# Optimization experiments

Hardware: AMD Instinct MI355X
Metric: run time of the kernel (lower is better)

The kernel has to match this reference:

```python
import jax, jax.numpy as jnp
import numpy as np

B, S, D = 4, 2048, 1024


def setup_inputs() -> dict:
    key = jax.random.key(0)
    k1, k2, k3, k4 = jax.random.split(key, 4)
    x = jax.random.normal(k1, (B, S, D), dtype=jnp.float32)
    # 'random_normal' keras initializer uses stddev=0.05
    w_keys = jax.random.normal(k2, (D, D), dtype=jnp.float32) * 0.05
    w_queries = jax.random.normal(k3, (D, D), dtype=jnp.float32) * 0.05
    w_values = jax.random.normal(k4, (D, D), dtype=jnp.float32) * 0.05
    return {"x": x, "w_keys": w_keys, "w_queries": w_queries, "w_values": w_values}


def reference(x, w_keys, w_queries, w_values):
    # fact = sqrt(input feature dim)
    fact = jnp.sqrt(jnp.asarray(x.shape[-1], x.dtype))
    vk = x @ w_keys      # [B,S,D]
    vq = x @ w_queries   # [B,S,D]
    vv = x @ w_values    # [B,S,D]
    # NOTE: module computes K @ Q^T (keys as rows), softmax over last axis
    kq = jnp.einsum('bsd,btd->bst', vk, vq) / fact   # [B,S,S]
    sn = jax.nn.softmax(kq, axis=-1)
    # pm + transpose_b cancel: out = sn @ vv
    out = jnp.einsum('bst,btd->bsd', sn, vv)         # [B,S,D]
    return out
```

## Files before the change

kernel.cpp:

```cpp
#include <hip/hip_runtime.h>


typedef __attribute__((ext_vector_type(8))) short bf16x8;
typedef __attribute__((ext_vector_type(4))) float f32x4;

__device__ __forceinline__ unsigned short f2bf(float f) {
    unsigned int u = __float_as_uint(f);
    u += 0x7fff + ((u >> 16) & 1);
    return (unsigned short)(u >> 16);
}

__device__ __forceinline__ void gld_lds16(const unsigned short* g, unsigned short* l) {
    __builtin_amdgcn_global_load_lds(
        (const __attribute__((address_space(1))) void*)g,
        (__attribute__((address_space(3))) void*)l, 16, 0, 0);
}

template<int N> __device__ __forceinline__ void vmcnt_wait() {
    if constexpr (N == 0) asm volatile("s_waitcnt vmcnt(0)" ::: "memory");
    else if constexpr (N == 8) asm volatile("s_waitcnt vmcnt(8)" ::: "memory");
}
__device__ __forceinline__ void bar() {
    asm volatile("" ::: "memory");
    __builtin_amdgcn_s_barrier();
    asm volatile("" ::: "memory");
}

template<int KT, bool RS>
__device__ __forceinline__ void gemm4(
    const unsigned short* __restrict__ A, const unsigned short* __restrict__ B,
    int lda, int ldb, int bm, int bn,
    unsigned short* As, unsigned short* Bs,
    f32x4 (&acc)[4][4], f32x4 (&os)[4])
{
    const int tid  = threadIdx.x;
    const int lane = tid & 63;
    const int wave = tid >> 6;
    const int wr = wave >> 1, wc = wave & 1;
    const int lr = lane & 15, kg = lane >> 4;

    const bf16x8 ONES = { (short)0x3F80, (short)0x3F80, (short)0x3F80, (short)0x3F80,
                          (short)0x3F80, (short)0x3F80, (short)0x3F80, (short)0x3F80 };

    const int srow = tid >> 2;
    const int ssrc = ((tid & 3) ^ ((tid >> 3) & 3)) * 8;
    const unsigned short* pa0 = A + (size_t)(bm + srow) * lda + ssrc;
    const unsigned short* pa1 = A + (size_t)(bm + 64 + srow) * lda + ssrc;
    const unsigned short* pb0 = B + (size_t)(bn + srow) * ldb + ssrc;
    const unsigned short* pb1 = B + (size_t)(bn + 64 + srow) * ldb + ssrc;

    const int phys = (kg ^ ((lr >> 1) & 3)) * 8;
    const int aoff = (wr * 64 + lr) * 32 + phys;
    const int boff = (wc * 64 + lr) * 32 + phys;

    auto stage = [&](int buf, int kt) {
        unsigned short* da = As + buf * 8192 + wave * 512;
        unsigned short* db = Bs + buf * 8192 + wave * 512;
        #pragma unroll
        for (int kh = 0; kh < 2; kh++) {
            const int go = kt * 64 + kh * 32;
            gld_lds16(pa0 + go, da + kh * 4096);
            gld_lds16(pa1 + go, da + kh * 4096 + 2048);
            gld_lds16(pb0 + go, db + kh * 4096);
            gld_lds16(pb1 + go, db + kh * 4096 + 2048);
        }
    };

    stage(0, 0);
    stage(1, 1);
    vmcnt_wait<8>();
    bar();

    for (int kt = 0; kt < KT; ++kt) {
        const int c = kt & 1;
        const unsigned short* Ab = As + c * 8192 + aoff;
        const unsigned short* Bb = Bs + c * 8192 + boff;

        #pragma unroll
        for (int kh = 0; kh < 2; kh++) {
            bf16x8 af[4], bf[4];
            #pragma unroll
            for (int mf = 0; mf < 4; mf++)
                af[mf] = *reinterpret_cast<const bf16x8*>(Ab + kh * 4096 + mf * 512);
            #pragma unroll
            for (int nf = 0; nf < 4; nf++)
                bf[nf] = *reinterpret_cast<const bf16x8*>(Bb + kh * 4096 + nf * 512);
            __builtin_amdgcn_s_setprio(1);
            #pragma unroll
            for (int mf = 0; mf < 4; mf++)
                #pragma unroll
                for (int nf = 0; nf < 4; nf++)
                    acc[mf][nf] = __builtin_amdgcn_mfma_f32_16x16x32_bf16(af[mf], bf[nf], acc[mf][nf], 0, 0, 0);
            if constexpr (RS) {
                #pragma unroll
                for (int mf = 0; mf < 4; mf++)
                    os[mf] = __builtin_amdgcn_mfma_f32_16x16x32_bf16(af[mf], ONES, os[mf], 0, 0, 0);
            }
            __builtin_amdgcn_s_setprio(0);
        }

        if (kt == KT - 1) break;
        bar();
        if (kt + 2 < KT) {
            stage(c, kt + 2);
            vmcnt_wait<8>();
        } else {
            vmcnt_wait<0>();
        }
        bar();
    }
}

__global__ __launch_bounds__(256) void stage1(
    const float* __restrict__ x,  unsigned short* __restrict__ xb,
    const float* __restrict__ wv, unsigned short* __restrict__ wvT,
    const float* __restrict__ wq, const float* __restrict__ wk,
    unsigned short* __restrict__ Gt)
{
    __shared__ unsigned short SM[4608];
    const int bid = blockIdx.x;
    const int tid = threadIdx.x;

    if (bid >= 256 && bid < 4352) {
        const size_t idx = (size_t)(bid - 256) * 256 + tid;
        const float4* xi = reinterpret_cast<const float4*>(x) + idx * 2;
        float4 v0 = xi[0], v1 = xi[1];
        ushort4 a = { f2bf(v0.x), f2bf(v0.y), f2bf(v0.z), f2bf(v0.w) };
        ushort4 b = { f2bf(v1.x), f2bf(v1.y), f2bf(v1.z), f2bf(v1.w) };
        ushort4* xo = reinterpret_cast<ushort4*>(xb) + idx * 2;
        xo[0] = a; xo[1] = b;
        return;
    }
    if (bid >= 4352) {
        auto T = reinterpret_cast<unsigned short (*)[72]>(SM);
        const int tb = bid - 4352;
        const int k0 = (tb >> 4) * 64, n0 = (tb & 15) * 64;
        const int r = tid >> 4, c4 = (tid & 15) * 4;
        #pragma unroll
        for (int i = 0; i < 4; i++) {
            int kr = r + i * 16;
            float4 v = *reinterpret_cast<const float4*>(&wv[(size_t)(k0 + kr) * 1024 + n0 + c4]);
            T[c4 + 0][kr] = f2bf(v.x);
            T[c4 + 1][kr] = f2bf(v.y);
            T[c4 + 2][kr] = f2bf(v.z);
            T[c4 + 3][kr] = f2bf(v.w);
        }
        __syncthreads();
        #pragma unroll
        for (int i = 0; i < 4; i++) {
            int n = r + i * 16;
            ushort4 v = *reinterpret_cast<const ushort4*>(&T[n][c4]);
            *reinterpret_cast<ushort4*>(&wvT[(size_t)(n0 + n) * 1024 + k0 + c4]) = v;
        }
        return;
    }

    unsigned short* As = SM;
    unsigned short* Bs = SM + 2048;
    const int gb = bid;
    const int bm = (gb >> 4) * 64, bn = (gb & 15) * 64;

    const int lane = tid & 63;
    const int wave = tid >> 6;
    const int wr = wave >> 1, wc = wave & 1;
    const int lr = lane & 15, kg = lane >> 4;

    const int srow = tid >> 2;
    const int su   = tid & 3;
    const int sphys = (su ^ ((srow >> 1) & 3)) * 8;
    const int rphys = (kg ^ ((lr >> 1) & 3)) * 8;
    const int aoff = (wr * 32 + lr) * 32 + rphys;
    const int boff = (wc * 32 + lr) * 32 + rphys;

    const float* pa = &wq[(size_t)(bm + srow) * 1024 + su * 8];
    const float* pb = &wk[(size_t)(bn + srow) * 1024 + su * 8];

    f32x4 acc[2][2] = {};

    float4 a0 = *reinterpret_cast<const float4*>(pa);
    float4 a1 = *reinterpret_cast<const float4*>(pa + 4);
    float4 b0 = *reinterpret_cast<const float4*>(pb);
    float4 b1 = *reinterpret_cast<const float4*>(pb + 4);

    for (int k0 = 0; k0 < 1024; k0 += 32) {
        ushort4 u0 = { f2bf(a0.x), f2bf(a0.y), f2bf(a0.z), f2bf(a0.w) };
        ushort4 u1 = { f2bf(a1.x), f2bf(a1.y), f2bf(a1.z), f2bf(a1.w) };
        *reinterpret_cast<ushort4*>(&As[srow * 32 + sphys])     = u0;
        *reinterpret_cast<ushort4*>(&As[srow * 32 + sphys + 4]) = u1;
        ushort4 t0 = { f2bf(b0.x), f2bf(b0.y), f2bf(b0.z), f2bf(b0.w) };
        ushort4 t1 = { f2bf(b1.x), f2bf(b1.y), f2bf(b1.z), f2bf(b1.w) };
        *reinterpret_cast<ushort4*>(&Bs[srow * 32 + sphys])     = t0;
        *reinterpret_cast<ushort4*>(&Bs[srow * 32 + sphys + 4]) = t1;

        if (k0 + 32 < 1024) {
            const float* npa = pa + k0 + 32;
            const float* npb = pb + k0 + 32;
            a0 = *reinterpret_cast<const float4*>(npa);
            a1 = *reinterpret_cast<const float4*>(npa + 4);
            b0 = *reinterpret_cast<const float4*>(npb);
            b1 = *reinterpret_cast<const float4*>(npb + 4);
        }
        __syncthreads();

        bf16x8 af[2], bf[2];
        #pragma unroll
        for (int mf = 0; mf < 2; mf++)
            af[mf] = *reinterpret_cast<const bf16x8*>(&As[aoff + mf * 512]);
        #pragma unroll
        for (int nf = 0; nf < 2; nf++)
            bf[nf] = *reinterpret_cast<const bf16x8*>(&Bs[boff + nf * 512]);
        #pragma unroll
        for (int mf = 0; mf < 2; mf++)
            #pragma unroll
            for (int nf = 0; nf < 2; nf++)
                acc[mf][nf] = __builtin_amdgcn_mfma_f32_16x16x32_bf16(af[mf], bf[nf], acc[mf][nf], 0, 0, 0);
        __syncthreads();
    }
    #pragma unroll
    for (int mf = 0; mf < 2; mf++)
        #pragma unroll
        for (int nf = 0; nf < 2; nf++)
            #pragma unroll
            for (int r = 0; r < 4; r++)
                Gt[(size_t)(bm + wr * 32 + mf * 16 + kg * 4 + r) * 1024
                   + bn + wc * 32 + nf * 16 + lr] = f2bf(acc[mf][nf][r]);
}

__global__ __launch_bounds__(256, 2) void proj_gemm(
    const unsigned short* __restrict__ xb, const unsigned short* __restrict__ Gt,
    const unsigned short* __restrict__ wvT,
    unsigned short* __restrict__ y, unsigned short* __restrict__ vvT)
{
    __shared__ unsigned short As[2 * 128 * 64], Bs[2 * 128 * 64];
    const int bid = blockIdx.x;
    const int wg  = (bid & 7) * 128 + (bid >> 3);
    const int z   = wg >> 9;
    const int rem = wg & 511;
    const int bm  = (rem >> 3) * 128;
    const int bn  = (rem & 7) * 128;
    const unsigned short* Bw = z ? wvT : Gt;

    f32x4 acc[4][4] = {};
    f32x4 os[4] = {};
    gemm4<16, false>(xb, Bw, 1024, 1024, bm, bn, As, Bs, acc, os);

    const int tid = threadIdx.x, lane = tid & 63, wave = tid >> 6;
    const int wr = wave >> 1, wc = wave & 1, lr = lane & 15, kg = lane >> 4;
    if (z == 0) {
        #pragma unroll
        for (int mf = 0; mf < 4; mf++)
            #pragma unroll
            for (int nf = 0; nf < 4; nf++)
                #pragma unroll
                for (int r = 0; r < 4; r++)
                    y[(size_t)(bm + wr * 64 + mf * 16 + kg * 4 + r) * 1024
                      + bn + wc * 64 + nf * 16 + lr] = f2bf(acc[mf][nf][r]);
    } else {
        const int batch = bm >> 11;
        unsigned short* o = vvT + (size_t)batch * 1024 * 2048;
        #pragma unroll
        for (int mf = 0; mf < 4; mf++)
            #pragma unroll
            for (int nf = 0; nf < 4; nf++) {
                ushort4 v = { f2bf(acc[mf][nf][0]), f2bf(acc[mf][nf][1]),
                              f2bf(acc[mf][nf][2]), f2bf(acc[mf][nf][3]) };
                *reinterpret_cast<ushort4*>(
                    &o[(size_t)(bn + wc * 64 + nf * 16 + lr) * 2048
                       + (bm & 2047) + wr * 64 + mf * 16 + kg * 4]) = v;
            }
    }
}

__global__ __launch_bounds__(256, 2) void scores_gemm(
    const unsigned short* __restrict__ y, const unsigned short* __restrict__ xb,
    unsigned short* __restrict__ P)
{
    __shared__ unsigned short As[2 * 128 * 64], Bs[2 * 128 * 64];
    const int bid = blockIdx.x;
    const int wg  = (bid & 7) * 128 + (bid >> 3);
    const int z   = wg >> 8;
    const int rem = wg & 255;
    const int bm  = (rem >> 4) * 128;
    const int bn  = (rem & 15) * 128;
    const unsigned short* A = y  + (size_t)z * 2048 * 1024;
    const unsigned short* B = xb + (size_t)z * 2048 * 1024;
    unsigned short* out = P + (size_t)z * 2048 * 2048;

    f32x4 acc[4][4] = {};
    f32x4 os[4] = {};
    gemm4<16, false>(A, B, 1024, 1024, bm, bn, As, Bs, acc, os);

    const int tid = threadIdx.x, lane = tid & 63, wave = tid >> 6;
    const int wr = wave >> 1, wc = wave & 1, lr = lane & 15, kg = lane >> 4;
    #pragma unroll
    for (int mf = 0; mf < 4; mf++)
        #pragma unroll
        for (int nf = 0; nf < 4; nf++)
            #pragma unroll
            for (int r = 0; r < 4; r++)
                out[(size_t)(bm + wr * 64 + mf * 16 + kg * 4 + r) * 2048
                    + bn + wc * 64 + nf * 16 + lr]
                    = f2bf(__expf(acc[mf][nf][r] * 0.03125f));
}

__global__ __launch_bounds__(256, 2) void pv_gemm(
    const unsigned short* __restrict__ P, const unsigned short* __restrict__ vvT,
    float* __restrict__ out)
{
    __shared__ unsigned short As[2 * 128 * 64], Bs[2 * 128 * 64];
    const int bid = blockIdx.x;
    const int wg  = (bid & 7) * 64 + (bid >> 3);
    const int z   = wg >> 7;
    const int rem = wg & 127;
    const int bm  = (rem >> 3) * 128;
    const int bn  = (rem & 7) * 128;
    const unsigned short* A = P   + (size_t)z * 2048 * 2048;
    const unsigned short* B = vvT + (size_t)z * 1024 * 2048;
    float* o = out + (size_t)z * 2048 * 1024;

    f32x4 acc[4][4] = {};
    f32x4 os[4] = {};
    gemm4<32, true>(A, B, 2048, 2048, bm, bn, As, Bs, acc, os);

    const int tid = threadIdx.x, lane = tid & 63, wave = tid >> 6;
    const int wr = wave >> 1, wc = wave & 1, lr = lane & 15, kg = lane >> 4;

    #pragma unroll
    for (int mf = 0; mf < 4; mf++)
        #pragma unroll
        for (int r = 0; r < 4; r++) {
            const float inv = 1.0f / os[mf][r];
            #pragma unroll
            for (int nf = 0; nf < 4; nf++)
                o[(size_t)(bm + wr * 64 + mf * 16 + kg * 4 + r) * 1024
                  + bn + wc * 64 + nf * 16 + lr] = acc[mf][nf][r] * inv;
        }
}

extern "C" void kernel_launch(void* const* d_in, const int* in_sizes, int n_in,
                              void* d_out, int out_size, void* d_ws, size_t ws_size,
                              hipStream_t stream) {
    const float* x  = (const float*)d_in[0];
    const float* wk = (const float*)d_in[1];
    const float* wq = (const float*)d_in[2];
    const float* wv = (const float*)d_in[3];
    float* out = (float*)d_out;

    char* ws = (char*)d_ws;
    const size_t MB = 1024 * 1024;
    unsigned short* xb  = (unsigned short*)(ws);
    unsigned short* y   = (unsigned short*)(ws + 16 * MB);
    unsigned short* Gt  = (unsigned short*)(ws + 32 * MB);
    unsigned short* wvT = (unsigned short*)(ws + 34 * MB);
    unsigned short* vvT = (unsigned short*)(ws + 36 * MB);
    unsigned short* P   = (unsigned short*)(ws + 52 * MB);

    stage1     <<<dim3(4608), 256, 0, stream>>>(x, xb, wv, wvT, wq, wk, Gt);
    proj_gemm  <<<dim3(1024), 256, 0, stream>>>(xb, Gt, wvT, y, vvT);
    scores_gemm<<<dim3(1024), 256, 0, stream>>>(y, xb, P);
    pv_gemm    <<<dim3(512),  256, 0, stream>>>(P, vvT, out);
}
```

Before: 156.0 us.

## Switch GEMMs to 256x256 tiles with 8 waves and interleaved staging

Replaces the 4-wave 128x128 GEMM core with an 8-wave 256-row tile (256 or 128 columns). The K step grows to 64, and the global-to-LDS loads for the next tile are split across the four MFMA phases, with a barrier after each phase. The larger tiles are meant to raise data reuse per LDS load and overlap the copies with compute. In exchange, register pressure per wave rises, LDS use grows to 128KB for some kernels, fewer workgroups are launched (256 on a 256-CU part), and there are more barriers per K step.

```diff
diff --git a/kernel.cpp b/kernel.cpp
--- a/kernel.cpp
+++ b/kernel.cpp
@@ -18,7 +18,7 @@
 
 template<int N> __device__ __forceinline__ void vmcnt_wait() {
     if constexpr (N == 0) asm volatile("s_waitcnt vmcnt(0)" ::: "memory");
-    else if constexpr (N == 8) asm volatile("s_waitcnt vmcnt(8)" ::: "memory");
+    else if constexpr (N == 2) asm volatile("s_waitcnt vmcnt(2)" ::: "memory");
 }
 __device__ __forceinline__ void bar() {
     asm volatile("" ::: "memory");
@@ -26,88 +26,98 @@
     asm volatile("" ::: "memory");
 }
 
-template<int KT, bool RS>
-__device__ __forceinline__ void gemm4(
+template<int NFR, int KT, bool RS>
+__device__ __forceinline__ void gemm8w(
     const unsigned short* __restrict__ A, const unsigned short* __restrict__ B,
     int lda, int ldb, int bm, int bn,
     unsigned short* As, unsigned short* Bs,
-    f32x4 (&acc)[4][4], f32x4 (&os)[4])
-{
+    f32x4 (&acc)[8][NFR], f32x4 (&os)[8])
+{
+    constexpr int NH    = NFR / 2;
+    constexpr int BROWS = NFR * 64;
+    constexpr int NS    = 2 + BROWS / 128;
     const int tid  = threadIdx.x;
     const int lane = tid & 63;
     const int wave = tid >> 6;
-    const int wr = wave >> 1, wc = wave & 1;
+    const int wr = wave >> 2, wc = wave & 3;
     const int lr = lane & 15, kg = lane >> 4;
 
     const bf16x8 ONES = { (short)0x3F80, (short)0x3F80, (short)0x3F80, (short)0x3F80,
                           (short)0x3F80, (short)0x3F80, (short)0x3F80, (short)0x3F80 };
 
-    const int srow = tid >> 2;
-    const int ssrc = ((tid & 3) ^ ((tid >> 3) & 3)) * 8;
-    const unsigned short* pa0 = A + (size_t)(bm + srow) * lda + ssrc;
-    const unsigned short* pa1 = A + (size_t)(bm + 64 + srow) * lda + ssrc;
-    const unsigned short* pb0 = B + (size_t)(bn + srow) * ldb + ssrc;
-    const unsigned short* pb1 = B + (size_t)(bn + 64 + srow) * ldb + ssrc;
-
-    const int phys = (kg ^ ((lr >> 1) & 3)) * 8;
-    const int aoff = (wr * 64 + lr) * 32 + phys;
-    const int boff = (wc * 64 + lr) * 32 + phys;
-
-    auto stage = [&](int buf, int kt) {
-        unsigned short* da = As + buf * 8192 + wave * 512;
-        unsigned short* db = Bs + buf * 8192 + wave * 512;
-        #pragma unroll
-        for (int kh = 0; kh < 2; kh++) {
-            const int go = kt * 64 + kh * 32;
-            gld_lds16(pa0 + go, da + kh * 4096);
-            gld_lds16(pa1 + go, da + kh * 4096 + 2048);
-            gld_lds16(pb0 + go, db + kh * 4096);
-            gld_lds16(pb1 + go, db + kh * 4096 + 2048);
+    const int ssrc = ((tid & 7) ^ ((tid >> 3) & 7)) * 8;
+    const unsigned short* gA = A + (size_t)(bm + (tid >> 3)) * lda + ssrc;
+    const unsigned short* gB = B + (size_t)(bn + (tid >> 3)) * ldb + ssrc;
+    unsigned short* dA = As + wave * 512;
+    unsigned short* dB = Bs + wave * 512;
+
+    auto sev = [&](int buf, int kt, int e) {
+        if (e < 2) {
+            const unsigned short* s = gA + ((size_t)e * 128) * lda + kt * 64;
+            unsigned short* d = dA + buf * 16384 + e * 8192;
+            gld_lds16(s, d);
+            gld_lds16(s + (size_t)64 * lda, d + 4096);
+        } else {
+            const int h = e - 2;
+            const unsigned short* s = gB + ((size_t)h * 128) * ldb + kt * 64;
+            unsigned short* d = dB + buf * (BROWS * 64) + h * 8192;
+            gld_lds16(s, d);
+            gld_lds16(s + (size_t)64 * ldb, d + 4096);
         }
     };
 
-    stage(0, 0);
-    stage(1, 1);
-    vmcnt_wait<8>();
-    bar();
+    const int arow = (wr * 128 + lr) * 64;
+    const int brow = (wc * (BROWS / 4) + lr) * 64;
+
+    #pragma unroll
+    for (int e = 0; e < NS; e++) sev(0, 0, e);
 
     for (int kt = 0; kt < KT; ++kt) {
-        const int c = kt & 1;
-        const unsigned short* Ab = As + c * 8192 + aoff;
-        const unsigned short* Bb = Bs + c * 8192 + boff;
-
-        #pragma unroll
-        for (int kh = 0; kh < 2; kh++) {
-            bf16x8 af[4], bf[4];
-            #pragma unroll
-            for (int mf = 0; mf < 4; mf++)
-                af[mf] = *reinterpret_cast<const bf16x8*>(Ab + kh * 4096 + mf * 512);
-            #pragma unroll
-            for (int nf = 0; nf < 4; nf++)
-                bf[nf] = *reinterpret_cast<const bf16x8*>(Bb + kh * 4096 + nf * 512);
+        const int c = kt & 1, n = c ^ 1;
+        const bool last = (kt == KT - 1);
+        const unsigned short* Ab = As + c * 16384 + arow;
+        const unsigned short* Bb = Bs + c * (BROWS * 64) + brow;
+
+        bf16x8 af[8], bfr[NH];
+        #pragma unroll
+        for (int p = 0; p < 4; ++p) {
+            const int kk = p >> 1, nfh = p & 1;
+            const int phys = ((kk * 4 + kg) ^ (lr & 7)) * 8;
+
+            if (p == 0) {
+                if (!last) { sev(n, kt + 1, 0); vmcnt_wait<2>(); }
+                else       { vmcnt_wait<0>(); }
+                bar();
+            }
+            if (nfh == 0) {
+                #pragma unroll
+                for (int mf = 0; mf < 8; mf++)
+                    af[mf] = *reinterpret_cast<const bf16x8*>(Ab + mf * 1024 + phys);
+            }
+            #pragma unroll
+            for (int j = 0; j < NH; j++)
+                bfr[j] = *reinterpret_cast<const bf16x8*>(Bb + (nfh * NH + j) * 1024 + phys);
+            if (p > 0) {
+                if (p < NS && !last) sev(n, kt + 1, p);
+                bar();
+            }
             __builtin_amdgcn_s_setprio(1);
             #pragma unroll
-            for (int mf = 0; mf < 4; mf++)
+            for (int mf = 0; mf < 8; mf++)
                 #pragma unroll
-                for (int nf = 0; nf < 4; nf++)
-                    acc[mf][nf] = __builtin_amdgcn_mfma_f32_16x16x32_bf16(af[mf], bf[nf], acc[mf][nf], 0, 0, 0);
+                for (int j = 0; j < NH; j++)
+                    acc[mf][nfh * NH + j] =
+                        __builtin_amdgcn_mfma_f32_16x16x32_bf16(af[mf], bfr[j], acc[mf][nfh * NH + j], 0, 0, 0);
             if constexpr (RS) {
-                #pragma unroll
-                for (int mf = 0; mf < 4; mf++)
-                    os[mf] = __builtin_amdgcn_mfma_f32_16x16x32_bf16(af[mf], ONES, os[mf], 0, 0, 0);
+                if (nfh == 0) {
+                    #pragma unroll
+                    for (int mf = 0; mf < 8; mf++)
+                        os[mf] = __builtin_amdgcn_mfma_f32_16x16x32_bf16(af[mf], ONES, os[mf], 0, 0, 0);
+                }
             }
             __builtin_amdgcn_s_setprio(0);
-        }
-
-        if (kt == KT - 1) break;
-        bar();
-        if (kt + 2 < KT) {
-            stage(c, kt + 2);
-            vmcnt_wait<8>();
-        } else {
-            vmcnt_wait<0>();
-        }
-        bar();
+            bar();
+        }
     }
 }
 
@@ -226,114 +236,114 @@
                    + bn + wc * 32 + nf * 16 + lr] = f2bf(acc[mf][nf][r]);
 }
 
-__global__ __launch_bounds__(256, 2) void proj_gemm(
+__global__ __launch_bounds__(512, 2) void proj_gemm(
     const unsigned short* __restrict__ xb, const unsigned short* __restrict__ Gt,
     const unsigned short* __restrict__ wvT,
     unsigned short* __restrict__ y, unsigned short* __restrict__ vvT)
 {
-    __shared__ unsigned short As[2 * 128 * 64], Bs[2 * 128 * 64];
+    __shared__ unsigned short As[2 * 256 * 64], Bs[2 * 256 * 64];
     const int bid = blockIdx.x;
-    const int wg  = (bid & 7) * 128 + (bid >> 3);
-    const int z   = wg >> 9;
-    const int rem = wg & 511;
-    const int bm  = (rem >> 3) * 128;
-    const int bn  = (rem & 7) * 128;
+    const int wg  = (bid & 7) * 32 + (bid >> 3);
+    const int z   = wg >> 7;
+    const int rem = wg & 127;
+    const int bm  = (rem >> 2) * 256;
+    const int bn  = (rem & 3) * 256;
     const unsigned short* Bw = z ? wvT : Gt;
 
-    f32x4 acc[4][4] = {};
-    f32x4 os[4] = {};
-    gemm4<16, false>(xb, Bw, 1024, 1024, bm, bn, As, Bs, acc, os);
+    f32x4 acc[8][4] = {};
+    f32x4 os[8];
+    gemm8w<4, 16, false>(xb, Bw, 1024, 1024, bm, bn, As, Bs, acc, os);
 
     const int tid = threadIdx.x, lane = tid & 63, wave = tid >> 6;
-    const int wr = wave >> 1, wc = wave & 1, lr = lane & 15, kg = lane >> 4;
+    const int wr = wave >> 2, wc = wave & 3, lr = lane & 15, kg = lane >> 4;
     if (z == 0) {
         #pragma unroll
-        for (int mf = 0; mf < 4; mf++)
+        for (int mf = 0; mf < 8; mf++)
             #pragma unroll
             for (int nf = 0; nf < 4; nf++)
                 #pragma unroll
                 for (int r = 0; r < 4; r++)
-                    y[(size_t)(bm + wr * 64 + mf * 16 + kg * 4 + r) * 1024
+                    y[(size_t)(bm + wr * 128 + mf * 16 + kg * 4 + r) * 1024
                       + bn + wc * 64 + nf * 16 + lr] = f2bf(acc[mf][nf][r]);
     } else {
         const int batch = bm >> 11;
         unsigned short* o = vvT + (size_t)batch * 1024 * 2048;
         #pragma unroll
-        for (int mf = 0; mf < 4; mf++)
+        for (int mf = 0; mf < 8; mf++)
             #pragma unroll
             for (int nf = 0; nf < 4; nf++) {
                 ushort4 v = { f2bf(acc[mf][nf][0]), f2bf(acc[mf][nf][1]),
                               f2bf(acc[mf][nf][2]), f2bf(acc[mf][nf][3]) };
                 *reinterpret_cast<ushort4*>(
                     &o[(size_t)(bn + wc * 64 + nf * 16 + lr) * 2048
-                       + (bm & 2047) + wr * 64 + mf * 16 + kg * 4]) = v;
-            }
-    }
-}
-
-__global__ __launch_bounds__(256, 2) void scores_gemm(
+                       + (bm & 2047) + wr * 128 + mf * 16 + kg * 4]) = v;
+            }
+    }
+}
+
+__global__ __launch_bounds__(512, 2) void scores_gemm(
     const unsigned short* __restrict__ y, const unsigned short* __restrict__ xb,
     unsigned short* __restrict__ P)
 {
-    __shared__ unsigned short As[2 * 128 * 64], Bs[2 * 128 * 64];
+    __shared__ unsigned short As[2 * 256 * 64], Bs[2 * 256 * 64];
     const int bid = blockIdx.x;
-    const int wg  = (bid & 7) * 128 + (bid >> 3);
-    const int z   = wg >> 8;
-    const int rem = wg & 255;
-    const int bm  = (rem >> 4) * 128;
-    const int bn  = (rem & 15) * 128;
+    const int wg  = (bid & 7) * 32 + (bid >> 3);
+    const int z   = wg >> 6;
+    const int rem = wg & 63;
+    const int bm  = (rem >> 3) * 256;
+    const int bn  = (rem & 7) * 256;
     const unsigned short* A = y  + (size_t)z * 2048 * 1024;
     const unsigned short* B = xb + (size_t)z * 2048 * 1024;
     unsigned short* out = P + (size_t)z * 2048 * 2048;
 
-    f32x4 acc[4][4] = {};
-    f32x4 os[4] = {};
-    gemm4<16, false>(A, B, 1024, 1024, bm, bn, As, Bs, acc, os);
+    f32x4 acc[8][4] = {};
+    f32x4 os[8];
+    gemm8w<4, 16, false>(A, B, 1024, 1024, bm, bn, As, Bs, acc, os);
 
     const int tid = threadIdx.x, lane = tid & 63, wave = tid >> 6;
-    const int wr = wave >> 1, wc = wave & 1, lr = lane & 15, kg = lane >> 4;
+    const int wr = wave >> 2, wc = wave & 3, lr = lane & 15, kg = lane >> 4;
     #pragma unroll
-    for (int mf = 0; mf < 4; mf++)
+    for (int mf = 0; mf < 8; mf++)
         #pragma unroll
         for (int nf = 0; nf < 4; nf++)
             #pragma unroll
             for (int r = 0; r < 4; r++)
-                out[(size_t)(bm + wr * 64 + mf * 16 + kg * 4 + r) * 2048
+                out[(size_t)(bm + wr * 128 + mf * 16 + kg * 4 + r) * 2048
                     + bn + wc * 64 + nf * 16 + lr]
                     = f2bf(__expf(acc[mf][nf][r] * 0.03125f));
 }
 
-__global__ __launch_bounds__(256, 2) void pv_gemm(
+__global__ __launch_bounds__(512, 2) void pv_gemm(
     const unsigned short* __restrict__ P, const unsigned short* __restrict__ vvT,
     float* __restrict__ out)
 {
-    __shared__ unsigned short As[2 * 128 * 64], Bs[2 * 128 * 64];
+    __shared__ unsigned short As[2 * 256 * 64], Bs[2 * 128 * 64];
     const int bid = blockIdx.x;
-    const int wg  = (bid & 7) * 64 + (bid >> 3);
-    const int z   = wg >> 7;
-    const int rem = wg & 127;
-    const int bm  = (rem >> 3) * 128;
+    const int wg  = (bid & 7) * 32 + (bid >> 3);
+    const int z   = wg >> 6;
+    const int rem = wg & 63;
+    const int bm  = (rem >> 3) * 256;
     const int bn  = (rem & 7) * 128;
     const unsigned short* A = P   + (size_t)z * 2048 * 2048;
     const unsigned short* B = vvT + (size_t)z * 1024 * 2048;
     float* o = out + (size_t)z * 2048 * 1024;
 
-    f32x4 acc[4][4] = {};
-    f32x4 os[4] = {};
-    gemm4<32, true>(A, B, 2048, 2048, bm, bn, As, Bs, acc, os);
+    f32x4 acc[8][2] = {};
+    f32x4 os[8] = {};
+    gemm8w<2, 32, true>(A, B, 2048, 2048, bm, bn, As, Bs, acc, os);
 
     const int tid = threadIdx.x, lane = tid & 63, wave = tid >> 6;
-    const int wr = wave >> 1, wc = wave & 1, lr = lane & 15, kg = lane >> 4;
+    const int wr = wave >> 2, wc = wave & 3, lr = lane & 15, kg = lane >> 4;
 
     #pragma unroll
-    for (int mf = 0; mf < 4; mf++)
+    for (int mf = 0; mf < 8; mf++)
         #pragma unroll
         for (int r = 0; r < 4; r++) {
             const float inv = 1.0f / os[mf][r];
             #pragma unroll
-            for (int nf = 0; nf < 4; nf++)
-                o[(size_t)(bm + wr * 64 + mf * 16 + kg * 4 + r) * 1024
-                  + bn + wc * 64 + nf * 16 + lr] = acc[mf][nf][r] * inv;
+            for (int nf = 0; nf < 2; nf++)
+                o[(size_t)(bm + wr * 128 + mf * 16 + kg * 4 + r) * 1024
+                  + bn + wc * 32 + nf * 16 + lr] = acc[mf][nf][r] * inv;
         }
 }
 
@@ -356,7 +366,7 @@
     unsigned short* P   = (unsigned short*)(ws + 52 * MB);
 
     stage1     <<<dim3(4608), 256, 0, stream>>>(x, xb, wv, wvT, wq, wk, Gt);
-    proj_gemm  <<<dim3(1024), 256, 0, stream>>>(xb, Gt, wvT, y, vvT);
-    scores_gemm<<<dim3(1024), 256, 0, stream>>>(y, xb, P);
-    pv_gemm    <<<dim3(512),  256, 0, stream>>>(P, vvT, out);
-}
+    proj_gemm  <<<dim3(256),  512, 0, stream>>>(xb, Gt, wvT, y, vvT);
+    scores_gemm<<<dim3(256),  512, 0, stream>>>(y, xb, P);
+    pv_gemm    <<<dim3(256),  512, 0, stream>>>(P, vvT, out);
+}
```

Measured after the change: 172.3 us. 1.1x slower.

## Load B operand directly from global into registers, keep only A in LDS

Applied to the files above, without the earlier changes.

The shared GEMM helper stops staging the B tile through LDS. Each wave now loads its B fragments straight from global memory into registers, double-buffered across k-steps, while A keeps its LDS double buffer. The loop is unrolled by two with adjusted vmcnt waits. This halves LDS footprint and LDS read traffic, which could allow more occupancy. The cost is that the two waves sharing a column each load the same B data redundantly, and register pressure rises from holding two B fragment sets.

```diff
diff --git a/kernel.cpp b/kernel.cpp
--- a/kernel.cpp
+++ b/kernel.cpp
@@ -17,8 +17,9 @@
 }
 
 template<int N> __device__ __forceinline__ void vmcnt_wait() {
-    if constexpr (N == 0) asm volatile("s_waitcnt vmcnt(0)" ::: "memory");
-    else if constexpr (N == 8) asm volatile("s_waitcnt vmcnt(8)" ::: "memory");
+    if constexpr (N == 0)  asm volatile("s_waitcnt vmcnt(0)"  ::: "memory");
+    else if constexpr (N == 8)  asm volatile("s_waitcnt vmcnt(8)"  ::: "memory");
+    else if constexpr (N == 12) asm volatile("s_waitcnt vmcnt(12)" ::: "memory");
 }
 __device__ __forceinline__ void bar() {
     asm volatile("" ::: "memory");
@@ -27,12 +28,13 @@
 }
 
 template<int KT, bool RS>
-__device__ __forceinline__ void gemm4(
+__device__ __forceinline__ void gemm4b(
     const unsigned short* __restrict__ A, const unsigned short* __restrict__ B,
     int lda, int ldb, int bm, int bn,
-    unsigned short* As, unsigned short* Bs,
+    unsigned short* As,
     f32x4 (&acc)[4][4], f32x4 (&os)[4])
 {
+    static_assert(KT % 2 == 0, "KT must be even");
     const int tid  = threadIdx.x;
     const int lane = tid & 63;
     const int wave = tid >> 6;
@@ -46,51 +48,51 @@
     const int ssrc = ((tid & 3) ^ ((tid >> 3) & 3)) * 8;
     const unsigned short* pa0 = A + (size_t)(bm + srow) * lda + ssrc;
     const unsigned short* pa1 = A + (size_t)(bm + 64 + srow) * lda + ssrc;
-    const unsigned short* pb0 = B + (size_t)(bn + srow) * ldb + ssrc;
-    const unsigned short* pb1 = B + (size_t)(bn + 64 + srow) * ldb + ssrc;
 
     const int phys = (kg ^ ((lr >> 1) & 3)) * 8;
     const int aoff = (wr * 64 + lr) * 32 + phys;
-    const int boff = (wc * 64 + lr) * 32 + phys;
-
-    auto stage = [&](int buf, int kt) {
+
+    const unsigned short* pB0 = B + (size_t)(bn + wc * 64 +  0 + lr) * ldb + kg * 8;
+    const unsigned short* pB1 = B + (size_t)(bn + wc * 64 + 16 + lr) * ldb + kg * 8;
+    const unsigned short* pB2 = B + (size_t)(bn + wc * 64 + 32 + lr) * ldb + kg * 8;
+    const unsigned short* pB3 = B + (size_t)(bn + wc * 64 + 48 + lr) * ldb + kg * 8;
+
+    auto stageA = [&](int buf, int kt) {
         unsigned short* da = As + buf * 8192 + wave * 512;
-        unsigned short* db = Bs + buf * 8192 + wave * 512;
         #pragma unroll
         for (int kh = 0; kh < 2; kh++) {
             const int go = kt * 64 + kh * 32;
             gld_lds16(pa0 + go, da + kh * 4096);
             gld_lds16(pa1 + go, da + kh * 4096 + 2048);
-            gld_lds16(pb0 + go, db + kh * 4096);
-            gld_lds16(pb1 + go, db + kh * 4096 + 2048);
         }
     };
 
-    stage(0, 0);
-    stage(1, 1);
-    vmcnt_wait<8>();
-    bar();
-
-    for (int kt = 0; kt < KT; ++kt) {
-        const int c = kt & 1;
-        const unsigned short* Ab = As + c * 8192 + aoff;
-        const unsigned short* Bb = Bs + c * 8192 + boff;
-
+    typedef bf16x8 Bfrag[4][2];
+    auto loadB = [&](Bfrag& d, int kt) {
         #pragma unroll
         for (int kh = 0; kh < 2; kh++) {
-            bf16x8 af[4], bf[4];
+            const int go = kt * 64 + kh * 32;
+            d[0][kh] = *reinterpret_cast<const bf16x8*>(pB0 + go);
+            d[1][kh] = *reinterpret_cast<const bf16x8*>(pB1 + go);
+            d[2][kh] = *reinterpret_cast<const bf16x8*>(pB2 + go);
+            d[3][kh] = *reinterpret_cast<const bf16x8*>(pB3 + go);
+        }
+    };
+
+    auto comp = [&](int buf, Bfrag& bf) {
+        const unsigned short* Ab = As + buf * 8192 + aoff;
+        #pragma unroll
+        for (int kh = 0; kh < 2; kh++) {
+            bf16x8 af[4];
             #pragma unroll
             for (int mf = 0; mf < 4; mf++)
                 af[mf] = *reinterpret_cast<const bf16x8*>(Ab + kh * 4096 + mf * 512);
-            #pragma unroll
-            for (int nf = 0; nf < 4; nf++)
-                bf[nf] = *reinterpret_cast<const bf16x8*>(Bb + kh * 4096 + nf * 512);
             __builtin_amdgcn_s_setprio(1);
             #pragma unroll
             for (int mf = 0; mf < 4; mf++)
                 #pragma unroll
                 for (int nf = 0; nf < 4; nf++)
-                    acc[mf][nf] = __builtin_amdgcn_mfma_f32_16x16x32_bf16(af[mf], bf[nf], acc[mf][nf], 0, 0, 0);
+                    acc[mf][nf] = __builtin_amdgcn_mfma_f32_16x16x32_bf16(af[mf], bf[nf][kh], acc[mf][nf], 0, 0, 0);
             if constexpr (RS) {
                 #pragma unroll
                 for (int mf = 0; mf < 4; mf++)
@@ -98,15 +100,31 @@
             }
             __builtin_amdgcn_s_setprio(0);
         }
-
-        if (kt == KT - 1) break;
+    };
+
+    Bfrag b0, b1;
+
+    stageA(0, 0);
+    stageA(1, 1);
+    loadB(b0, 0);
+    vmcnt_wait<12>();
+    bar();
+
+    for (int kt = 0; kt < KT; kt += 2) {
+        if (kt + 1 < KT) loadB(b1, kt + 1);
+        comp(0, b0);
         bar();
-        if (kt + 2 < KT) {
-            stage(c, kt + 2);
-            vmcnt_wait<8>();
-        } else {
-            vmcnt_wait<0>();
-        }
+        if (kt + 2 < KT) { stageA(0, kt + 2); vmcnt_wait<12>(); }
+        else             { vmcnt_wait<8>(); }
+        bar();
+
+        const int k1 = kt + 1;
+        if (k1 + 1 < KT) loadB(b0, k1 + 1);
+        comp(1, b1);
+        if (k1 == KT - 1) break;
+        bar();
+        stageA(1, k1 + 2);
+        vmcnt_wait<12>();
         bar();
     }
 }
@@ -231,7 +249,7 @@
     const unsigned short* __restrict__ wvT,
     unsigned short* __restrict__ y, unsigned short* __restrict__ vvT)
 {
-    __shared__ unsigned short As[2 * 128 * 64], Bs[2 * 128 * 64];
+    __shared__ unsigned short As[2 * 128 * 64];
     const int bid = blockIdx.x;
     const int wg  = (bid & 7) * 128 + (bid >> 3);
     const int z   = wg >> 9;
@@ -242,7 +260,7 @@
 
     f32x4 acc[4][4] = {};
     f32x4 os[4] = {};
-    gemm4<16, false>(xb, Bw, 1024, 1024, bm, bn, As, Bs, acc, os);
+    gemm4b<16, false>(xb, Bw, 1024, 1024, bm, bn, As, acc, os);
 
     const int tid = threadIdx.x, lane = tid & 63, wave = tid >> 6;
     const int wr = wave >> 1, wc = wave & 1, lr = lane & 15, kg = lane >> 4;
@@ -275,7 +293,7 @@
     const unsigned short* __restrict__ y, const unsigned short* __restrict__ xb,
     unsigned short* __restrict__ P)
 {
-    __shared__ unsigned short As[2 * 128 * 64], Bs[2 * 128 * 64];
+    __shared__ unsigned short As[2 * 128 * 64];
     const int bid = blockIdx.x;
     const int wg  = (bid & 7) * 128 + (bid >> 3);
     const int z   = wg >> 8;
@@ -288,7 +306,7 @@
 
     f32x4 acc[4][4] = {};
     f32x4 os[4] = {};
-    gemm4<16, false>(A, B, 1024, 1024, bm, bn, As, Bs, acc, os);
+    gemm4b<16, false>(A, B, 1024, 1024, bm, bn, As, acc, os);
 
     const int tid = threadIdx.x, lane = tid & 63, wave = tid >> 6;
     const int wr = wave >> 1, wc = wave & 1, lr = lane & 15, kg = lane >> 4;
@@ -307,7 +325,7 @@
     const unsigned short* __restrict__ P, const unsigned short* __restrict__ vvT,
     float* __restrict__ out)
 {
-    __shared__ unsigned short As[2 * 128 * 64], Bs[2 * 128 * 64];
+    __shared__ unsigned short As[2 * 128 * 64];
     const int bid = blockIdx.x;
     const int wg  = (bid & 7) * 64 + (bid >> 3);
     const int z   = wg >> 7;
@@ -320,7 +338,7 @@
 
     f32x4 acc[4][4] = {};
     f32x4 os[4] = {};
-    gemm4<32, true>(A, B, 2048, 2048, bm, bn, As, Bs, acc, os);
+    gemm4b<32, true>(A, B, 2048, 2048, bm, bn, As, acc, os);
 
     const int tid = threadIdx.x, lane = tid & 63, wave = tid >> 6;
     const int wr = wave >> 1, wc = wave & 1, lr = lane & 15, kg = lane >> 4;
```

Result: slower. 251.1 us (+61.0%).

## Give each wave private LDS tiles and drop block barriers in GEMM mainloop

Applied to the files above, without the earlier changes.

The shared GEMM core now has each wave load its own 64-row slices of A and B into a private LDS region (128KB per block), with a new XOR swizzle. Waves synchronise only through their own vmcnt/lgkmcnt waits, so the s_barrier calls between stages go away. The cost is that rows shared across waves are loaded redundantly, doubling global/L2 traffic. The larger LDS footprint also drops occupancy to one block per CU, so the launch bounds lose their min-blocks hint.

```diff
diff --git a/kernel.cpp b/kernel.cpp
--- a/kernel.cpp
+++ b/kernel.cpp
@@ -17,20 +17,18 @@
 }
 
 template<int N> __device__ __forceinline__ void vmcnt_wait() {
-    if constexpr (N == 0) asm volatile("s_waitcnt vmcnt(0)" ::: "memory");
-    else if constexpr (N == 8) asm volatile("s_waitcnt vmcnt(8)" ::: "memory");
-}
-__device__ __forceinline__ void bar() {
-    asm volatile("" ::: "memory");
-    __builtin_amdgcn_s_barrier();
-    asm volatile("" ::: "memory");
+    if constexpr (N == 0)  asm volatile("s_waitcnt vmcnt(0)"  ::: "memory");
+    else if constexpr (N == 16) asm volatile("s_waitcnt vmcnt(16)" ::: "memory");
+}
+__device__ __forceinline__ void lgkm0() {
+    asm volatile("s_waitcnt lgkmcnt(0)" ::: "memory");
 }
 
 template<int KT, bool RS>
-__device__ __forceinline__ void gemm4(
+__device__ __forceinline__ void gemm4p(
     const unsigned short* __restrict__ A, const unsigned short* __restrict__ B,
     int lda, int ldb, int bm, int bn,
-    unsigned short* As, unsigned short* Bs,
+    unsigned short* Ls,
     f32x4 (&acc)[4][4], f32x4 (&os)[4])
 {
     const int tid  = threadIdx.x;
@@ -42,49 +40,38 @@
     const bf16x8 ONES = { (short)0x3F80, (short)0x3F80, (short)0x3F80, (short)0x3F80,
                           (short)0x3F80, (short)0x3F80, (short)0x3F80, (short)0x3F80 };
 
-    const int srow = tid >> 2;
-    const int ssrc = ((tid & 3) ^ ((tid >> 3) & 3)) * 8;
-    const unsigned short* pa0 = A + (size_t)(bm + srow) * lda + ssrc;
-    const unsigned short* pa1 = A + (size_t)(bm + 64 + srow) * lda + ssrc;
-    const unsigned short* pb0 = B + (size_t)(bn + srow) * ldb + ssrc;
-    const unsigned short* pb1 = B + (size_t)(bn + 64 + srow) * ldb + ssrc;
-
-    const int phys = (kg ^ ((lr >> 1) & 3)) * 8;
-    const int aoff = (wr * 64 + lr) * 32 + phys;
-    const int boff = (wc * 64 + lr) * 32 + phys;
+    unsigned short* reg0 = Ls + wave * 16384;
+
+    const int srl = lane >> 3;
+    const int gsu = (lane & 7) ^ srl;
+    const unsigned short* ga = A + (size_t)(bm + wr * 64 + srl) * lda + gsu * 8;
+    const unsigned short* gb = B + (size_t)(bn + wc * 64 + srl) * ldb + gsu * 8;
 
     auto stage = [&](int buf, int kt) {
-        unsigned short* da = As + buf * 8192 + wave * 512;
-        unsigned short* db = Bs + buf * 8192 + wave * 512;
+        unsigned short* da = reg0 + buf * 8192;
+        unsigned short* db = da + 4096;
+        const int go = kt * 64;
+        #pragma unroll
+        for (int i = 0; i < 8; i++)
+            gld_lds16(ga + (size_t)(i * 8) * lda + go, da + i * 512);
+        #pragma unroll
+        for (int i = 0; i < 8; i++)
+            gld_lds16(gb + (size_t)(i * 8) * ldb + go, db + i * 512);
+    };
+
+    auto comp = [&](int buf) {
+        const unsigned short* Ab = reg0 + buf * 8192;
+        const unsigned short* Bb = Ab + 4096;
         #pragma unroll
         for (int kh = 0; kh < 2; kh++) {
-            const int go = kt * 64 + kh * 32;
-            gld_lds16(pa0 + go, da + kh * 4096);
-            gld_lds16(pa1 + go, da + kh * 4096 + 2048);
-            gld_lds16(pb0 + go, db + kh * 4096);
-            gld_lds16(pb1 + go, db + kh * 4096 + 2048);
-        }
-    };
-
-    stage(0, 0);
-    stage(1, 1);
-    vmcnt_wait<8>();
-    bar();
-
-    for (int kt = 0; kt < KT; ++kt) {
-        const int c = kt & 1;
-        const unsigned short* Ab = As + c * 8192 + aoff;
-        const unsigned short* Bb = Bs + c * 8192 + boff;
-
-        #pragma unroll
-        for (int kh = 0; kh < 2; kh++) {
+            const int pu = (((kh * 4) + kg) ^ (lr & 7)) * 8;
             bf16x8 af[4], bf[4];
             #pragma unroll
             for (int mf = 0; mf < 4; mf++)
-                af[mf] = *reinterpret_cast<const bf16x8*>(Ab + kh * 4096 + mf * 512);
+                af[mf] = *reinterpret_cast<const bf16x8*>(Ab + (mf * 16 + lr) * 64 + pu);
             #pragma unroll
             for (int nf = 0; nf < 4; nf++)
-                bf[nf] = *reinterpret_cast<const bf16x8*>(Bb + kh * 4096 + nf * 512);
+                bf[nf] = *reinterpret_cast<const bf16x8*>(Bb + (nf * 16 + lr) * 64 + pu);
             __builtin_amdgcn_s_setprio(1);
             #pragma unroll
             for (int mf = 0; mf < 4; mf++)
@@ -98,16 +85,22 @@
             }
             __builtin_amdgcn_s_setprio(0);
         }
-
+    };
+
+    stage(0, 0);
+    stage(1, 1);
+    vmcnt_wait<16>();
+
+    for (int kt = 0; kt < KT; ++kt) {
+        comp(kt & 1);
         if (kt == KT - 1) break;
-        bar();
+        lgkm0();
         if (kt + 2 < KT) {
-            stage(c, kt + 2);
-            vmcnt_wait<8>();
+            stage(kt & 1, kt + 2);
+            vmcnt_wait<16>();
         } else {
             vmcnt_wait<0>();
         }
-        bar();
     }
 }
 
@@ -226,12 +219,12 @@
                    + bn + wc * 32 + nf * 16 + lr] = f2bf(acc[mf][nf][r]);
 }
 
-__global__ __launch_bounds__(256, 2) void proj_gemm(
+__global__ __launch_bounds__(256) void proj_gemm(
     const unsigned short* __restrict__ xb, const unsigned short* __restrict__ Gt,
     const unsigned short* __restrict__ wvT,
     unsigned short* __restrict__ y, unsigned short* __restrict__ vvT)
 {
-    __shared__ unsigned short As[2 * 128 * 64], Bs[2 * 128 * 64];
+    __shared__ unsigned short Ls[65536];
     const int bid = blockIdx.x;
     const int wg  = (bid & 7) * 128 + (bid >> 3);
     const int z   = wg >> 9;
@@ -242,7 +235,7 @@
 
     f32x4 acc[4][4] = {};
     f32x4 os[4] = {};
-    gemm4<16, false>(xb, Bw, 1024, 1024, bm, bn, As, Bs, acc, os);
+    gemm4p<16, false>(xb, Bw, 1024, 1024, bm, bn, Ls, acc, os);
 
     const int tid = threadIdx.x, lane = tid & 63, wave = tid >> 6;
     const int wr = wave >> 1, wc = wave & 1, lr = lane & 15, kg = lane >> 4;
@@ -271,11 +264,11 @@
     }
 }
 
-__global__ __launch_bounds__(256, 2) void scores_gemm(
+__global__ __launch_bounds__(256) void scores_gemm(
     const unsigned short* __restrict__ y, const unsigned short* __restrict__ xb,
     unsigned short* __restrict__ P)
 {
-    __shared__ unsigned short As[2 * 128 * 64], Bs[2 * 128 * 64];
+    __shared__ unsigned short Ls[65536];
     const int bid = blockIdx.x;
     const int wg  = (bid & 7) * 128 + (bid >> 3);
     const int z   = wg >> 8;
@@ -288,7 +281,7 @@
 
     f32x4 acc[4][4] = {};
     f32x4 os[4] = {};
-    gemm4<16, false>(A, B, 1024, 1024, bm, bn, As, Bs, acc, os);
+    gemm4p<16, false>(A, B, 1024, 1024, bm, bn, Ls, acc, os);
 
     const int tid = threadIdx.x, lane = tid & 63, wave = tid >> 6;
     const int wr = wave >> 1, wc = wave & 1, lr = lane & 15, kg = lane >> 4;
@@ -303,11 +296,11 @@
                     = f2bf(__expf(acc[mf][nf][r] * 0.03125f));
 }
 
-__global__ __launch_bounds__(256, 2) void pv_gemm(
+__global__ __launch_bounds__(256) void pv_gemm(
     const unsigned short* __restrict__ P, const unsigned short* __restrict__ vvT,
     float* __restrict__ out)
 {
-    __shared__ unsigned short As[2 * 128 * 64], Bs[2 * 128 * 64];
+    __shared__ unsigned short Ls[65536];
     const int bid = blockIdx.x;
     const int wg  = (bid & 7) * 64 + (bid >> 3);
     const int z   = wg >> 7;
@@ -320,7 +313,7 @@
 
     f32x4 acc[4][4] = {};
     f32x4 os[4] = {};
-    gemm4<32, true>(A, B, 2048, 2048, bm, bn, As, Bs, acc, os);
+    gemm4p<32, true>(A, B, 2048, 2048, bm, bn, Ls, acc, os);
 
     const int tid = threadIdx.x, lane = tid & 63, wave = tid >> 6;
     const int wr = wave >> 1, wc = wave & 1, lr = lane & 15, kg = lane >> 4;
```

Measured after the change: 195.0 us. 1.25x slower.
